# Kernel optimization log

Measured on AMD Instinct MI355X. Metric: run time of the kernel, lower is better.

## Reference

```python
import jax, jax.numpy as jnp
import numpy as np

EPS = 1e-12
ALPHA = 0.2  # LeakyReLU negative slope
N_NODES = 100000
N_EDGES = 1600000
F = 128
H = 8

def setup_inputs() -> dict:
    key = jax.random.key(0)
    k1, k2, k3, k4 = jax.random.split(key, 4)
    x = jax.random.normal(k1, (N_NODES, F), dtype=jnp.float32)
    row = jax.random.randint(k2, (N_EDGES,), 0, N_NODES, dtype=jnp.int32)
    col = jax.random.randint(k3, (N_EDGES,), 0, N_NODES, dtype=jnp.int32)
    # xavier_uniform with gain=1.414 on [H, 2F]
    limit = 1.414 * np.sqrt(6.0 / (H + 2 * F))
    aa = jax.random.uniform(k4, (H, 2 * F), dtype=jnp.float32, minval=-limit, maxval=limit)
    return {"x": x, "row": row, "col": col, "aa": aa}

def reference(x, row, col, aa):
    # e = leakyrelu(aa @ cat(x[row], x[col], dim=1).T)  -> [H, E]
    # Split aa so per-node scores are computed once, then gathered per edge
    # (identical math, avoids materializing the [E, 2F] concat).
    a_src, a_dst = aa[:, :F], aa[:, F:]          # [H, F] each
    s_src = x @ a_src.T                           # [N, H]
    s_dst = x @ a_dst.T                           # [N, H]
    e = s_src[row] + s_dst[col]                   # [E, H]
    e = jnp.where(e > 0, e, ALPHA * e)            # LeakyReLU
    # scatter_softmax over edges grouped by row (per head)
    m = jax.ops.segment_max(e, row, num_segments=N_NODES)  # [N, H]
    m = jnp.where(jnp.isfinite(m), m, 0.0)        # empty segments -> -inf; neutralize
    ex = jnp.exp(e - m[row])                      # [E, H]
    s = jax.ops.segment_sum(ex, row, num_segments=N_NODES)  # [N, H]
    a = ex / (s[row] + EPS)                       # [E, H]
    return a.T                                    # [H, E] to match torch layout
```

## Files before the change

kernel.cpp:

```cpp
#include <hip/hip_runtime.h>

constexpr int N_NODES = 100000;
constexpr int N_EDGES = 1600000;
constexpr int F = 128;
constexpr int H = 8;
constexpr float ALPHA = 0.2f;
constexpr float EPSF = 1e-12f;

constexpr int PSHIFT = 8;
constexpr int PN = 1 << PSHIFT;
constexpr int NPART = (N_NODES + PN - 1) / PN;
constexpr int MAXPART = 5120;
constexpr int EPB = 4096;
constexpr int OCAP = 4096;

static_assert(N_EDGES % 64 == 0, "k4_hs assumes 64-edge blocks");

__global__ void k1_scores(const float* __restrict__ x, const float* __restrict__ aa,
                          float* __restrict__ srn, float* __restrict__ sd) {
    __shared__ float sa[H * 2 * F];
    for (int i = threadIdx.x; i < H * 2 * F; i += blockDim.x) sa[i] = aa[i];
    __syncthreads();
    int node = blockIdx.x * blockDim.x + threadIdx.x;
    if (node >= N_NODES) return;
    const float4* xr = reinterpret_cast<const float4*>(x + (size_t)node * F);
    float accs[H], accd[H];
#pragma unroll
    for (int h = 0; h < H; ++h) { accs[h] = 0.f; accd[h] = 0.f; }
    for (int f4 = 0; f4 < F / 4; ++f4) {
        float4 xv = xr[f4];
#pragma unroll
        for (int h = 0; h < H; ++h) {
            float4 av = *reinterpret_cast<const float4*>(&sa[h * 2 * F + 4 * f4]);
            float4 bv = *reinterpret_cast<const float4*>(&sa[h * 2 * F + F + 4 * f4]);
            accs[h] += xv.x * av.x + xv.y * av.y + xv.z * av.z + xv.w * av.w;
            accd[h] += xv.x * bv.x + xv.y * bv.y + xv.z * bv.z + xv.w * bv.w;
        }
    }
    float4* os = reinterpret_cast<float4*>(srn + (size_t)node * 16);
    os[0] = make_float4(accs[0], accs[1], accs[2], accs[3]);
    os[1] = make_float4(accs[4], accs[5], accs[6], accs[7]);
    float4* od = reinterpret_cast<float4*>(sd + (size_t)node * H);
    od[0] = make_float4(accd[0], accd[1], accd[2], accd[3]);
    od[1] = make_float4(accd[4], accd[5], accd[6], accd[7]);
}

__global__ void __launch_bounds__(1024)
kA_part(const int* __restrict__ row, const int* __restrict__ col,
        int* __restrict__ gcnt, unsigned* __restrict__ part,
        int* __restrict__ ocnt, int2* __restrict__ olist) {
    __shared__ int hist[NPART];
    __shared__ int base[NPART];
    const int t = threadIdx.x;
    const int e0 = blockIdx.x * EPB;
    constexpr int K = EPB / 1024;
    int rr[K], cc[K];
    for (int p = t; p < NPART; p += 1024) hist[p] = 0;
    __syncthreads();
#pragma unroll
    for (int k = 0; k < K; ++k) {
        int i = e0 + k * 1024 + t;
        if (i < N_EDGES) {
            rr[k] = row[i];
            cc[k] = col[i];
            atomicAdd(&hist[rr[k] >> PSHIFT], 1);
        } else rr[k] = -1;
    }
    __syncthreads();
    for (int p = t; p < NPART; p += 1024) {
        int h = hist[p];
        base[p] = h ? atomicAdd(&gcnt[p], h) : 0;
        hist[p] = 0;
    }
    __syncthreads();
#pragma unroll
    for (int k = 0; k < K; ++k) {
        if (rr[k] >= 0) {
            int r = rr[k], c = cc[k];
            int p = r >> PSHIFT;
            int slot = base[p] + atomicAdd(&hist[p], 1);
            unsigned pk = ((unsigned)(r & (PN - 1)) << 17) | (unsigned)c;
            if (slot < MAXPART) {
                part[(size_t)p * MAXPART + slot] = pk;
            } else {
                int q = atomicAdd(ocnt, 1);
                if (q < OCAP) olist[q] = make_int2(p, (int)pk);
            }
        }
    }
}

__global__ void __launch_bounds__(1024)
kB_sum(const float* __restrict__ sd, const unsigned* __restrict__ part,
       const int* __restrict__ gcnt, const int* __restrict__ ocnt,
       const int2* __restrict__ olist, float* __restrict__ srn) {
    __shared__ unsigned plist[MAXPART];
    __shared__ unsigned sorted_c[MAXPART];
    __shared__ int hist[PN];
    __shared__ int off[PN + 1];
    __shared__ int cur[PN];
    __shared__ float ssrc[PN * H];
    const int p = blockIdx.x;
    const int t = threadIdx.x;
    const int nbase = p << PSHIFT;

    for (int i = t; i < PN; i += 1024) hist[i] = 0;
    for (int j = t; j < PN * H; j += 1024) {
        int n = nbase + (j >> 3);
        ssrc[j] = (n < N_NODES) ? srn[(size_t)n * 16 + (j & 7)] : 0.f;
    }
    __syncthreads();

    int cnt = gcnt[p]; if (cnt > MAXPART) cnt = MAXPART;
    const unsigned* pp = part + (size_t)p * MAXPART;

    for (int i = t; i < cnt; i += 1024) {
        unsigned pk = pp[i];
        plist[i] = pk;
        atomicAdd(&hist[pk >> 17], 1);
    }
    __syncthreads();

    for (int d = 1; d < PN; d <<= 1) {
        int add = 0;
        if (t >= d && t < PN) add = hist[t - d];
        __syncthreads();
        if (t < PN) hist[t] += add;
        __syncthreads();
    }
    if (t < PN) off[t + 1] = hist[t];
    if (t == 0) off[0] = 0;
    __syncthreads();
    if (t < PN) cur[t] = off[t];
    __syncthreads();

    for (int i = t; i < cnt; i += 1024) {
        unsigned pk = plist[i];
        int rl = (int)(pk >> 17);
        int slot = atomicAdd(&cur[rl], 1);
        sorted_c[slot] = pk & 0x1FFFFu;
    }
    __syncthreads();

    int mo = *ocnt; if (mo > OCAP) mo = OCAP;
    {
        int nl = t >> 2, pi = t & 3;
        int node = nbase + nl;
        int k0 = off[nl], k1e = off[nl + 1];
        float s0 = ssrc[nl * 8 + 2 * pi];
        float s1 = ssrc[nl * 8 + 2 * pi + 1];
        float a0 = 0.f, a1 = 0.f;
        int k = k0;
        for (; k + 4 <= k1e; k += 4) {
            int c0 = (int)sorted_c[k],     c1 = (int)sorted_c[k + 1];
            int c2 = (int)sorted_c[k + 2], c3 = (int)sorted_c[k + 3];
            float2 d0 = *reinterpret_cast<const float2*>(&sd[(size_t)c0 * H + 2 * pi]);
            float2 d1 = *reinterpret_cast<const float2*>(&sd[(size_t)c1 * H + 2 * pi]);
            float2 d2 = *reinterpret_cast<const float2*>(&sd[(size_t)c2 * H + 2 * pi]);
            float2 d3 = *reinterpret_cast<const float2*>(&sd[(size_t)c3 * H + 2 * pi]);
            float e;
            e = s0 + d0.x; e = e > 0.f ? e : ALPHA * e; a0 += __expf(e);
            e = s1 + d0.y; e = e > 0.f ? e : ALPHA * e; a1 += __expf(e);
            e = s0 + d1.x; e = e > 0.f ? e : ALPHA * e; a0 += __expf(e);
            e = s1 + d1.y; e = e > 0.f ? e : ALPHA * e; a1 += __expf(e);
            e = s0 + d2.x; e = e > 0.f ? e : ALPHA * e; a0 += __expf(e);
            e = s1 + d2.y; e = e > 0.f ? e : ALPHA * e; a1 += __expf(e);
            e = s0 + d3.x; e = e > 0.f ? e : ALPHA * e; a0 += __expf(e);
            e = s1 + d3.y; e = e > 0.f ? e : ALPHA * e; a1 += __expf(e);
        }
        for (; k < k1e; ++k) {
            int c = (int)sorted_c[k];
            float2 d = *reinterpret_cast<const float2*>(&sd[(size_t)c * H + 2 * pi]);
            float e0 = s0 + d.x; e0 = e0 > 0.f ? e0 : ALPHA * e0;
            float e1 = s1 + d.y; e1 = e1 > 0.f ? e1 : ALPHA * e1;
            a0 += __expf(e0); a1 += __expf(e1);
        }
        for (int j = 0; j < mo; ++j) {
            int2 oe = olist[j];
            if (oe.x == p && (int)(((unsigned)oe.y) >> 17) == nl) {
                int c = oe.y & 0x1FFFF;
                float2 d = *reinterpret_cast<const float2*>(&sd[(size_t)c * H + 2 * pi]);
                float e0 = s0 + d.x; e0 = e0 > 0.f ? e0 : ALPHA * e0;
                float e1 = s1 + d.y; e1 = e1 > 0.f ? e1 : ALPHA * e1;
                a0 += __expf(e0); a1 += __expf(e1);
            }
        }
        if (node < N_NODES) {
            srn[(size_t)node * 16 + 8 + 2 * pi]     = 1.f / (a0 + EPSF);
            srn[(size_t)node * 16 + 8 + 2 * pi + 1] = 1.f / (a1 + EPSF);
        }
    }
}

__global__ void __launch_bounds__(512)
k4_hs(const int* __restrict__ row, const int* __restrict__ col,
      const float* __restrict__ srn, const float* __restrict__ sd,
      float* __restrict__ out) {
    __shared__ int ridx[64], cidx[64];
    __shared__ float sm[8][72];
    const int e0 = blockIdx.x * 64;
    const int t = threadIdx.x;
    if (t < 64) ridx[t] = row[e0 + t];
    else if (t < 128) cidx[t - 64] = col[e0 + t - 64];
    __syncthreads();
    {
        int el = t >> 3, h = t & 7;
        int r = ridx[el], c = cidx[el];
        float s  = srn[(size_t)r * 16 + h];
        float rv = srn[(size_t)r * 16 + 8 + h];
        float d  = sd[(size_t)c * H + h];
        float e = s + d;
        e = e > 0.f ? e : ALPHA * e;
        sm[h][el] = __expf(e) * rv;
    }
    __syncthreads();
    {
        int h2 = t >> 6, j = t & 63;
        out[(size_t)h2 * N_EDGES + e0 + j] = sm[h2][j];
    }
}

__global__ void kz_zero_sums(float* __restrict__ srn) {
    int t = blockIdx.x * blockDim.x + threadIdx.x;
    if (t >= N_NODES * H) return;
    srn[(size_t)(t >> 3) * 16 + 8 + (t & 7)] = 0.f;
}

__global__ void k3nm_sum(const float* __restrict__ srn_ro, const float* __restrict__ s_dst,
                         const int* __restrict__ row, const int* __restrict__ col,
                         float* __restrict__ srn) {
    int i = blockIdx.x * blockDim.x + threadIdx.x;
    if (i >= N_EDGES) return;
    int r = row[i], c = col[i];
    const float4* sr = reinterpret_cast<const float4*>(srn_ro + (size_t)r * 16);
    float4 a0 = sr[0], a1 = sr[1];
    const float4* sc = reinterpret_cast<const float4*>(s_dst + (size_t)c * H);
    float4 b0 = sc[0], b1 = sc[1];
    float ev[H] = {a0.x + b0.x, a0.y + b0.y, a0.z + b0.z, a0.w + b0.w,
                   a1.x + b1.x, a1.y + b1.y, a1.z + b1.z, a1.w + b1.w};
#pragma unroll
    for (int h = 0; h < H; ++h) {
        float e = ev[h] > 0.f ? ev[h] : ALPHA * ev[h];
        atomicAdd(&srn[(size_t)r * 16 + 8 + h], __expf(e));
    }
}

__global__ void k_inv(float* __restrict__ srn) {
    int t = blockIdx.x * blockDim.x + threadIdx.x;
    if (t >= N_NODES * H) return;
    int n = t >> 3, h = t & 7;
    float s = srn[(size_t)n * 16 + 8 + h];
    srn[(size_t)n * 16 + 8 + h] = 1.0f / (s + EPSF);
}

__global__ void k4_out(const int* __restrict__ row, const int* __restrict__ col,
                       const float* __restrict__ srn, const float* __restrict__ s_dst,
                       float* __restrict__ out) {
    int i = blockIdx.x * blockDim.x + threadIdx.x;
    if (i >= N_EDGES) return;
    int r = row[i], c = col[i];
    const float4* sr = reinterpret_cast<const float4*>(srn + (size_t)r * 16);
    float4 a0 = sr[0], a1 = sr[1], r0 = sr[2], r1 = sr[3];
    const float4* sc = reinterpret_cast<const float4*>(s_dst + (size_t)c * H);
    float4 b0 = sc[0], b1 = sc[1];
    float ev[H] = {a0.x + b0.x, a0.y + b0.y, a0.z + b0.z, a0.w + b0.w,
                   a1.x + b1.x, a1.y + b1.y, a1.z + b1.z, a1.w + b1.w};
    float rv[H] = {r0.x, r0.y, r0.z, r0.w, r1.x, r1.y, r1.z, r1.w};
#pragma unroll
    for (int h = 0; h < H; ++h) {
        float e = ev[h] > 0.f ? ev[h] : ALPHA * ev[h];
        out[(size_t)h * N_EDGES + i] = __expf(e) * rv[h];
    }
}

extern "C" void kernel_launch(void* const* d_in, const int* in_sizes, int n_in,
                              void* d_out, int out_size, void* d_ws, size_t ws_size,
                              hipStream_t stream) {
    const float* x   = (const float*)d_in[0];
    const int*   row = (const int*)d_in[1];
    const int*   col = (const int*)d_in[2];
    const float* aa  = (const float*)d_in[3];
    float* out = (float*)d_out;

    float*    srn  = (float*)d_ws;
    float*    sd   = srn + (size_t)N_NODES * 16;
    unsigned* part = (unsigned*)(sd + (size_t)N_NODES * H);
    int*      gcnt = (int*)(part + (size_t)NPART * MAXPART);
    int*      ocnt = gcnt + NPART;
    int2*     olist = (int2*)(ocnt + 16);

    const size_t need_b = ((size_t)N_NODES * 24 + (size_t)NPART * MAXPART
                           + NPART + 16 + 2 * OCAP) * 4;

    const int B = 256;
    const int GE  = (N_EDGES + B - 1) / B;
    const int GN  = (N_NODES + B - 1) / B;

    k1_scores<<<GN, B, 0, stream>>>(x, aa, srn, sd);

    if (ws_size >= need_b) {
        hipMemsetAsync(gcnt, 0, (size_t)(NPART + 16) * sizeof(int), stream);
        kA_part<<<(N_EDGES + EPB - 1) / EPB, 1024, 0, stream>>>(row, col, gcnt, part, ocnt, olist);
        kB_sum<<<NPART, 1024, 0, stream>>>(sd, part, gcnt, ocnt, olist, srn);
        k4_hs<<<N_EDGES / 64, 512, 0, stream>>>(row, col, srn, sd, out);
    } else {
        kz_zero_sums<<<(N_NODES * H + B - 1) / B, B, 0, stream>>>(srn);
        k3nm_sum<<<GE, B, 0, stream>>>(srn, sd, row, col, srn);
        k_inv<<<(N_NODES * H + B - 1) / B, B, 0, stream>>>(srn);
        k4_out<<<GE, B, 0, stream>>>(row, col, srn, sd, out);
    }
}
```

Baseline: 205.8 us.

## Fuse score computation and edge partitioning into one launch; warp-shuffle prefix scan

The per-node score GEMV and the edge-bucketing pass now run in a single kernel launch, split by block index, so the two independent phases overlap and one launch is removed. The score path moves to 1024-thread blocks and unrolls four float4 loads of x per iteration. In the per-partition sum kernel, the 256-entry prefix scan is replaced by a 64-lane shuffle scan over four elements per lane, which removes many block-wide barriers. The score branch now runs with 1024-thread blocks and higher register pressure, which may lower occupancy, and the fused blocks share one shared-memory footprint.

```diff
diff --git a/kernel.cpp b/kernel.cpp
--- a/kernel.cpp
+++ b/kernel.cpp
@@ -14,79 +14,99 @@
 constexpr int EPB = 4096;
 constexpr int OCAP = 4096;
 
+constexpr int KA_BLOCKS = (N_EDGES + EPB - 1) / EPB;
+constexpr int K1_BLOCKS = (N_NODES + 1023) / 1024;
+
 static_assert(N_EDGES % 64 == 0, "k4_hs assumes 64-edge blocks");
 
-__global__ void k1_scores(const float* __restrict__ x, const float* __restrict__ aa,
-                          float* __restrict__ srn, float* __restrict__ sd) {
-    __shared__ float sa[H * 2 * F];
-    for (int i = threadIdx.x; i < H * 2 * F; i += blockDim.x) sa[i] = aa[i];
-    __syncthreads();
-    int node = blockIdx.x * blockDim.x + threadIdx.x;
-    if (node >= N_NODES) return;
-    const float4* xr = reinterpret_cast<const float4*>(x + (size_t)node * F);
-    float accs[H], accd[H];
-#pragma unroll
-    for (int h = 0; h < H; ++h) { accs[h] = 0.f; accd[h] = 0.f; }
-    for (int f4 = 0; f4 < F / 4; ++f4) {
-        float4 xv = xr[f4];
-#pragma unroll
-        for (int h = 0; h < H; ++h) {
-            float4 av = *reinterpret_cast<const float4*>(&sa[h * 2 * F + 4 * f4]);
-            float4 bv = *reinterpret_cast<const float4*>(&sa[h * 2 * F + F + 4 * f4]);
-            accs[h] += xv.x * av.x + xv.y * av.y + xv.z * av.z + xv.w * av.w;
-            accd[h] += xv.x * bv.x + xv.y * bv.y + xv.z * bv.z + xv.w * bv.w;
-        }
-    }
-    float4* os = reinterpret_cast<float4*>(srn + (size_t)node * 16);
-    os[0] = make_float4(accs[0], accs[1], accs[2], accs[3]);
-    os[1] = make_float4(accs[4], accs[5], accs[6], accs[7]);
-    float4* od = reinterpret_cast<float4*>(sd + (size_t)node * H);
-    od[0] = make_float4(accd[0], accd[1], accd[2], accd[3]);
-    od[1] = make_float4(accd[4], accd[5], accd[6], accd[7]);
-}
-
 __global__ void __launch_bounds__(1024)
-kA_part(const int* __restrict__ row, const int* __restrict__ col,
-        int* __restrict__ gcnt, unsigned* __restrict__ part,
-        int* __restrict__ ocnt, int2* __restrict__ olist) {
+kA1_fused(const int* __restrict__ row, const int* __restrict__ col,
+          int* __restrict__ gcnt, unsigned* __restrict__ part,
+          int* __restrict__ ocnt, int2* __restrict__ olist,
+          const float* __restrict__ x, const float* __restrict__ aa,
+          float* __restrict__ srn, float* __restrict__ sd) {
     __shared__ int hist[NPART];
     __shared__ int base[NPART];
+    __shared__ float sa[H * 2 * F];
     const int t = threadIdx.x;
-    const int e0 = blockIdx.x * EPB;
-    constexpr int K = EPB / 1024;
-    int rr[K], cc[K];
-    for (int p = t; p < NPART; p += 1024) hist[p] = 0;
-    __syncthreads();
-#pragma unroll
-    for (int k = 0; k < K; ++k) {
-        int i = e0 + k * 1024 + t;
-        if (i < N_EDGES) {
-            rr[k] = row[i];
-            cc[k] = col[i];
-            atomicAdd(&hist[rr[k] >> PSHIFT], 1);
-        } else rr[k] = -1;
-    }
-    __syncthreads();
-    for (int p = t; p < NPART; p += 1024) {
-        int h = hist[p];
-        base[p] = h ? atomicAdd(&gcnt[p], h) : 0;
-        hist[p] = 0;
-    }
-    __syncthreads();
-#pragma unroll
-    for (int k = 0; k < K; ++k) {
-        if (rr[k] >= 0) {
-            int r = rr[k], c = cc[k];
-            int p = r >> PSHIFT;
-            int slot = base[p] + atomicAdd(&hist[p], 1);
-            unsigned pk = ((unsigned)(r & (PN - 1)) << 17) | (unsigned)c;
-            if (slot < MAXPART) {
-                part[(size_t)p * MAXPART + slot] = pk;
-            } else {
-                int q = atomicAdd(ocnt, 1);
-                if (q < OCAP) olist[q] = make_int2(p, (int)pk);
+
+    if (blockIdx.x < KA_BLOCKS) {
+        const int e0 = blockIdx.x * EPB;
+        constexpr int K = EPB / 1024;
+        int rr[K], cc[K];
+        for (int p = t; p < NPART; p += 1024) hist[p] = 0;
+        __syncthreads();
+#pragma unroll
+        for (int k = 0; k < K; ++k) {
+            int i = e0 + k * 1024 + t;
+            if (i < N_EDGES) {
+                rr[k] = row[i];
+                cc[k] = col[i];
+                atomicAdd(&hist[rr[k] >> PSHIFT], 1);
+            } else rr[k] = -1;
+        }
+        __syncthreads();
+        for (int p = t; p < NPART; p += 1024) {
+            int h = hist[p];
+            base[p] = h ? atomicAdd(&gcnt[p], h) : 0;
+            hist[p] = 0;
+        }
+        __syncthreads();
+#pragma unroll
+        for (int k = 0; k < K; ++k) {
+            if (rr[k] >= 0) {
+                int r = rr[k], c = cc[k];
+                int p = r >> PSHIFT;
+                int slot = base[p] + atomicAdd(&hist[p], 1);
+                unsigned pk = ((unsigned)(r & (PN - 1)) << 17) | (unsigned)c;
+                if (slot < MAXPART) {
+                    part[(size_t)p * MAXPART + slot] = pk;
+                } else {
+                    int q = atomicAdd(ocnt, 1);
+                    if (q < OCAP) olist[q] = make_int2(p, (int)pk);
+                }
             }
         }
+    } else {
+        if (t < 512) reinterpret_cast<float4*>(sa)[t] =
+            reinterpret_cast<const float4*>(aa)[t];
+        __syncthreads();
+        int node = (blockIdx.x - KA_BLOCKS) * 1024 + t;
+        if (node >= N_NODES) return;
+        const float4* xr = reinterpret_cast<const float4*>(x + (size_t)node * F);
+        float accs[H], accd[H];
+#pragma unroll
+        for (int h = 0; h < H; ++h) { accs[h] = 0.f; accd[h] = 0.f; }
+        for (int f4 = 0; f4 < F / 4; f4 += 4) {
+            float4 xv0 = xr[f4], xv1 = xr[f4 + 1], xv2 = xr[f4 + 2], xv3 = xr[f4 + 3];
+#pragma unroll
+            for (int h = 0; h < H; ++h) {
+                const float* ah = &sa[h * 2 * F + 4 * f4];
+                const float* bh = &sa[h * 2 * F + F + 4 * f4];
+                float4 a0 = *reinterpret_cast<const float4*>(ah);
+                float4 a1 = *reinterpret_cast<const float4*>(ah + 4);
+                float4 a2 = *reinterpret_cast<const float4*>(ah + 8);
+                float4 a3 = *reinterpret_cast<const float4*>(ah + 12);
+                accs[h] += xv0.x * a0.x + xv0.y * a0.y + xv0.z * a0.z + xv0.w * a0.w
+                         + xv1.x * a1.x + xv1.y * a1.y + xv1.z * a1.z + xv1.w * a1.w
+                         + xv2.x * a2.x + xv2.y * a2.y + xv2.z * a2.z + xv2.w * a2.w
+                         + xv3.x * a3.x + xv3.y * a3.y + xv3.z * a3.z + xv3.w * a3.w;
+                float4 b0 = *reinterpret_cast<const float4*>(bh);
+                float4 b1 = *reinterpret_cast<const float4*>(bh + 4);
+                float4 b2 = *reinterpret_cast<const float4*>(bh + 8);
+                float4 b3 = *reinterpret_cast<const float4*>(bh + 12);
+                accd[h] += xv0.x * b0.x + xv0.y * b0.y + xv0.z * b0.z + xv0.w * b0.w
+                         + xv1.x * b1.x + xv1.y * b1.y + xv1.z * b1.z + xv1.w * b1.w
+                         + xv2.x * b2.x + xv2.y * b2.y + xv2.z * b2.z + xv2.w * b2.w
+                         + xv3.x * b3.x + xv3.y * b3.y + xv3.z * b3.z + xv3.w * b3.w;
+            }
+        }
+        float4* os = reinterpret_cast<float4*>(srn + (size_t)node * 16);
+        os[0] = make_float4(accs[0], accs[1], accs[2], accs[3]);
+        os[1] = make_float4(accs[4], accs[5], accs[6], accs[7]);
+        float4* od = reinterpret_cast<float4*>(sd + (size_t)node * H);
+        od[0] = make_float4(accd[0], accd[1], accd[2], accd[3]);
+        od[1] = make_float4(accd[4], accd[5], accd[6], accd[7]);
     }
 }
 
@@ -121,17 +141,23 @@
     }
     __syncthreads();
 
-    for (int d = 1; d < PN; d <<= 1) {
-        int add = 0;
-        if (t >= d && t < PN) add = hist[t - d];
-        __syncthreads();
-        if (t < PN) hist[t] += add;
-        __syncthreads();
-    }
-    if (t < PN) off[t + 1] = hist[t];
-    if (t == 0) off[0] = 0;
-    __syncthreads();
-    if (t < PN) cur[t] = off[t];
+    if (t < 64) {
+        int h0 = hist[4 * t], h1 = hist[4 * t + 1];
+        int h2 = hist[4 * t + 2], h3 = hist[4 * t + 3];
+        int s0 = h0, s1 = s0 + h1, s2 = s1 + h2, s3 = s2 + h3;
+        int sc = s3;
+#pragma unroll
+        for (int d = 1; d < 64; d <<= 1) {
+            int v = __shfl_up(sc, d);
+            if (t >= d) sc += v;
+        }
+        int prefix = sc - s3;
+        off[4 * t + 1] = prefix + s0; off[4 * t + 2] = prefix + s1;
+        off[4 * t + 3] = prefix + s2; off[4 * t + 4] = prefix + s3;
+        cur[4 * t]     = prefix;      cur[4 * t + 1] = prefix + s0;
+        cur[4 * t + 2] = prefix + s1; cur[4 * t + 3] = prefix + s2;
+        if (t == 0) off[0] = 0;
+    }
     __syncthreads();
 
     for (int i = t; i < cnt; i += 1024) {
@@ -220,6 +246,35 @@
     }
 }
 
+__global__ void k1_scores(const float* __restrict__ x, const float* __restrict__ aa,
+                          float* __restrict__ srn, float* __restrict__ sd) {
+    __shared__ float sa[H * 2 * F];
+    for (int i = threadIdx.x; i < H * 2 * F; i += blockDim.x) sa[i] = aa[i];
+    __syncthreads();
+    int node = blockIdx.x * blockDim.x + threadIdx.x;
+    if (node >= N_NODES) return;
+    const float4* xr = reinterpret_cast<const float4*>(x + (size_t)node * F);
+    float accs[H], accd[H];
+#pragma unroll
+    for (int h = 0; h < H; ++h) { accs[h] = 0.f; accd[h] = 0.f; }
+    for (int f4 = 0; f4 < F / 4; ++f4) {
+        float4 xv = xr[f4];
+#pragma unroll
+        for (int h = 0; h < H; ++h) {
+            float4 av = *reinterpret_cast<const float4*>(&sa[h * 2 * F + 4 * f4]);
+            float4 bv = *reinterpret_cast<const float4*>(&sa[h * 2 * F + F + 4 * f4]);
+            accs[h] += xv.x * av.x + xv.y * av.y + xv.z * av.z + xv.w * av.w;
+            accd[h] += xv.x * bv.x + xv.y * bv.y + xv.z * bv.z + xv.w * bv.w;
+        }
+    }
+    float4* os = reinterpret_cast<float4*>(srn + (size_t)node * 16);
+    os[0] = make_float4(accs[0], accs[1], accs[2], accs[3]);
+    os[1] = make_float4(accs[4], accs[5], accs[6], accs[7]);
+    float4* od = reinterpret_cast<float4*>(sd + (size_t)node * H);
+    od[0] = make_float4(accd[0], accd[1], accd[2], accd[3]);
+    od[1] = make_float4(accd[4], accd[5], accd[6], accd[7]);
+}
+
 __global__ void kz_zero_sums(float* __restrict__ srn) {
     int t = blockIdx.x * blockDim.x + threadIdx.x;
     if (t >= N_NODES * H) return;
@@ -293,17 +348,17 @@
                            + NPART + 16 + 2 * OCAP) * 4;
 
     const int B = 256;
-    const int GE  = (N_EDGES + B - 1) / B;
-    const int GN  = (N_NODES + B - 1) / B;
-
-    k1_scores<<<GN, B, 0, stream>>>(x, aa, srn, sd);
+    const int GE = (N_EDGES + B - 1) / B;
+    const int GN = (N_NODES + B - 1) / B;
 
     if (ws_size >= need_b) {
         hipMemsetAsync(gcnt, 0, (size_t)(NPART + 16) * sizeof(int), stream);
-        kA_part<<<(N_EDGES + EPB - 1) / EPB, 1024, 0, stream>>>(row, col, gcnt, part, ocnt, olist);
+        kA1_fused<<<KA_BLOCKS + K1_BLOCKS, 1024, 0, stream>>>(
+            row, col, gcnt, part, ocnt, olist, x, aa, srn, sd);
         kB_sum<<<NPART, 1024, 0, stream>>>(sd, part, gcnt, ocnt, olist, srn);
         k4_hs<<<N_EDGES / 64, 512, 0, stream>>>(row, col, srn, sd, out);
     } else {
+        k1_scores<<<GN, B, 0, stream>>>(x, aa, srn, sd);
         kz_zero_sums<<<(N_NODES * H + B - 1) / B, B, 0, stream>>>(srn);
         k3nm_sum<<<GE, B, 0, stream>>>(srn, sd, row, col, srn);
         k_inv<<<(N_NODES * H + B - 1) / B, B, 0, stream>>>(srn);
```

Result: slower. 296.1 us (+43.9%).
